# Performance work log

Hardware: AMD Instinct MI355X
Metric: run time of the kernel (lower is better)

The kernel has to match this reference:

```python
import jax, jax.numpy as jnp
import numpy as np

TOP_K = 30
NUM_RBF = 16
NUM_POS = 16
MAX_REL = 32
EDGE_FEATURES = 128
EDGE_IN = NUM_POS + NUM_RBF * 9 + 7  # 167


def _normalize(x, axis=-1):
    # torch F.normalize: x / max(||x||, 1e-12)
    return x / jnp.maximum(jnp.linalg.norm(x, axis=axis, keepdims=True), 1e-12)


def _gather_nodes(nodes, idx):
    # nodes [B,L,C], idx [B,L,K] -> [B,L,K,C]
    return jax.vmap(lambda n, i: n[i])(nodes, idx)


def _rbf(D):
    D_mu = jnp.linspace(2.0, 22.0, NUM_RBF)  # [R]
    D_sigma = (22.0 - 2.0) / NUM_RBF
    return jnp.exp(-(((D[..., None] - D_mu) / D_sigma) ** 2))


def _get_rbf(A, B, E_idx):
    # full pairwise dist then gather neighbors (faithful to source)
    D_A_B = jnp.sqrt(jnp.sum((A[:, :, None, :] - B[:, None, :, :]) ** 2, -1) + 1e-6)
    D_nb = jnp.take_along_axis(D_A_B, E_idx, axis=2)  # [B,L,K]
    return _rbf(D_nb)


def _quaternions(R):
    # R [B,L,K,3,3] -> Q [B,L,K,4]
    diag = jnp.diagonal(R, axis1=-2, axis2=-1)  # [B,L,K,3]
    Rxx, Ryy, Rzz = diag[..., 0], diag[..., 1], diag[..., 2]
    magnitudes = 0.5 * jnp.sqrt(jnp.abs(1 + jnp.stack(
        [Rxx - Ryy - Rzz, -Rxx + Ryy - Rzz, -Rxx - Ryy + Rzz], -1)))
    signs = jnp.sign(jnp.stack([
        R[..., 2, 1] - R[..., 1, 2],
        R[..., 0, 2] - R[..., 2, 0],
        R[..., 1, 0] - R[..., 0, 1]], -1))
    xyz = signs * magnitudes
    w = jnp.sqrt(jax.nn.relu(1 + jnp.sum(diag, -1, keepdims=True))) / 2.0
    return _normalize(jnp.concatenate((xyz, w), -1))


def _orientations_coarse(X, E_idx, eps=1e-6):
    B, L, _ = X.shape
    dX = X[:, 1:, :] - X[:, :-1, :]
    dX_norm = jnp.linalg.norm(dX, axis=-1)
    dX_mask = (dX_norm > 3.6) & (dX_norm < 4.0)
    dX = dX * dX_mask[:, :, None]
    U = _normalize(dX)
    u_2, u_1, u_0 = U[:, :-2, :], U[:, 1:-1, :], U[:, 2:, :]
    n_2 = _normalize(jnp.cross(u_2, u_1))
    o_1 = _normalize(u_2 - u_1)
    # local frames O [B,L-3,3,3] -> flattened, padded to [B,L,9]
    O = jnp.stack((o_1, n_2, jnp.cross(o_1, n_2)), 2).reshape(B, L - 3, 9)
    O = jnp.pad(O, ((0, 0), (1, 2), (0, 0)))
    O_neighbors = _gather_nodes(O, E_idx)        # [B,L,K,9]
    X_neighbors = _gather_nodes(X, E_idx)        # [B,L,K,3]
    O = O.reshape(B, L, 3, 3)
    O_neighbors = O_neighbors.reshape(*E_idx.shape, 3, 3)
    dXn = X_neighbors - X[:, :, None, :]
    dU = _normalize(jnp.einsum('blij,blkj->blki', O, dXn))
    R = jnp.einsum('blji,blkjm->blkim', O, O_neighbors)  # O^T @ O_nb
    Q = _quaternions(R)
    return jnp.concatenate((dU, Q), -1)  # [B,L,K,7]


def setup_inputs() -> dict:
    B, L = 2, 4096
    key = jax.random.key(0)
    ks = jax.random.split(key, 6)
    Ca = jax.random.normal(ks[0], (B, L, 3), dtype=jnp.float32)
    mask = jnp.ones((B, L), dtype=jnp.float32)
    residue_idx = jnp.arange(B * L, dtype=jnp.int32).reshape(B, L)
    chain_labels = jnp.sort(jax.random.randint(ks[1], (B, L), 0, 4), axis=-1).astype(jnp.int32)
    pos_in = 2 * MAX_REL + 1 + 1  # 66
    pos_W = jax.random.normal(ks[2], (NUM_POS, pos_in), dtype=jnp.float32) / np.sqrt(pos_in)
    pos_b = jnp.zeros((NUM_POS,), dtype=jnp.float32)
    edge_W = jax.random.normal(ks[3], (EDGE_FEATURES, EDGE_IN), dtype=jnp.float32) / np.sqrt(EDGE_IN)
    ln_g = jnp.ones((EDGE_FEATURES,), dtype=jnp.float32)
    ln_b = jnp.zeros((EDGE_FEATURES,), dtype=jnp.float32)
    return {"Ca": Ca, "mask": mask, "residue_idx": residue_idx,
            "chain_labels": chain_labels, "pos_W": pos_W, "pos_b": pos_b,
            "edge_W": edge_W, "ln_g": ln_g, "ln_b": ln_b}


def _forward(Ca, mask, residue_idx, chain_labels, pos_W, pos_b, edge_W, ln_g, ln_b):
    B, L, _ = Ca.shape
    # _dist: masked pairwise distances + kNN
    mask_2D = mask[:, :, None] * mask[:, None, :]
    dX = Ca[:, None, :, :] - Ca[:, :, None, :]
    D = mask_2D * jnp.sqrt(jnp.sum(dX ** 2, 3) + 1e-6)
    D_max = jnp.max(D, -1, keepdims=True)
    D_adjust = D + (1.0 - mask_2D) * D_max
    k = min(TOP_K, L)
    neg_vals, E_idx = jax.lax.top_k(-D_adjust, k)  # smallest-k
    D_neighbors = -neg_vals

    zeros = jnp.zeros((B, 1, 3), dtype=Ca.dtype)
    Ca_0 = jnp.concatenate([zeros, Ca[:, :-1, :]], axis=1)
    Ca_1 = Ca
    Ca_2 = jnp.concatenate([Ca[:, 1:, :], zeros], axis=1)

    O_features = _orientations_coarse(Ca, E_idx)

    RBF_all = jnp.concatenate([
        _rbf(D_neighbors),
        _get_rbf(Ca_0, Ca_0, E_idx), _get_rbf(Ca_2, Ca_2, E_idx),
        _get_rbf(Ca_0, Ca_1, E_idx), _get_rbf(Ca_0, Ca_2, E_idx),
        _get_rbf(Ca_1, Ca_0, E_idx), _get_rbf(Ca_1, Ca_2, E_idx),
        _get_rbf(Ca_2, Ca_0, E_idx), _get_rbf(Ca_2, Ca_1, E_idx)], axis=-1)

    offset = residue_idx[:, :, None] - residue_idx[:, None, :]
    offset = jnp.take_along_axis(offset, E_idx, axis=2)  # [B,L,K]
    d_chains = (chain_labels[:, :, None] - chain_labels[:, None, :] == 0).astype(jnp.int32)
    E_chains = jnp.take_along_axis(d_chains, E_idx, axis=2)

    # PositionalEncodings
    d = jnp.clip(offset + MAX_REL, 0, 2 * MAX_REL) * E_chains + (1 - E_chains) * (2 * MAX_REL + 1)
    d_onehot = jax.nn.one_hot(d, 2 * MAX_REL + 2, dtype=jnp.float32)
    E_positional = d_onehot @ pos_W.T + pos_b

    E = jnp.concatenate((E_positional, RBF_all, O_features), -1)  # [B,L,K,167]
    E = E @ edge_W.T
    mu = jnp.mean(E, -1, keepdims=True)
    var = jnp.var(E, -1, keepdims=True)
    E = (E - mu) / jnp.sqrt(var + 1e-5) * ln_g + ln_b
    return E, E_idx


def reference(Ca, mask, residue_idx, chain_labels, pos_W, pos_b, edge_W, ln_g, ln_b):
    return _forward(Ca, mask, residue_idx, chain_labels, pos_W, pos_b, edge_W, ln_g, ln_b)
```

## Files before the change

### kernel.cpp

```cpp
#include <hip/hip_runtime.h>
#include <stdint.h>

#define LL 4096
#define NB 2
#define KK 30
#define CDIM 128
#define FROW 200

typedef _Float16 half_t;
typedef half_t half8 __attribute__((ext_vector_type(8)));
typedef float f32x4 __attribute__((ext_vector_type(4)));

__device__ __forceinline__ float3 loadCa(const float* __restrict__ Ca, int b, int idx) {
    const float* p = Ca + ((size_t)(b * LL + idx)) * 3;
    return make_float3(p[0], p[1], p[2]);
}
__device__ __forceinline__ float3 loadCa4(const f32x4* __restrict__ Ca4, int b, int idx) {
    f32x4 v = Ca4[b * LL + idx];
    return make_float3(v[0], v[1], v[2]);
}
__device__ __forceinline__ float3 shiftedCa4(const f32x4* __restrict__ Ca4, int b, int idx, int sel) {
    int jj = idx + sel - 1;
    if (jj < 0 || jj >= LL) return make_float3(0.f, 0.f, 0.f);
    return loadCa4(Ca4, b, jj);
}
__device__ __forceinline__ float sgnf(float x) { return (x > 0.f) ? 1.f : ((x < 0.f) ? -1.f : 0.f); }
__device__ __forceinline__ float pdist(float3 a, float3 c) {
    float dx = a.x - c.x, dy = a.y - c.y, dz = a.z - c.z;
    return sqrtf(dx * dx + dy * dy + dz * dz + 1e-6f);
}

__global__ __launch_bounds__(256) void prep_kernel(const float* __restrict__ W,
                                                   const float* __restrict__ posW,
                                                   const float* __restrict__ posb,
                                                   const float* __restrict__ Ca,
                                                   half_t* __restrict__ Bp,
                                                   half_t* __restrict__ pwt,
                                                   float* __restrict__ Of,
                                                   f32x4* __restrict__ Ca4) {
    int blk = blockIdx.x;
    int tid = threadIdx.x;
    if (blk < 12) {
        int idx = blk * 256 + tid;
        if (idx >= 8 * 6 * 64) return;
        int l = idx & 63;
        int ts = idx >> 6;
        int s = ts % 6, t = ts / 6;
        int n = 16 * t + (l & 15);
        int kbase = 32 * s + 8 * (l >> 4);
        half8 v;
#pragma unroll
        for (int e = 0; e < 8; e++) {
            int k = kbase + e;
            v[e] = (k < 167) ? (half_t)W[n * 167 + k] : (half_t)0.f;
        }
        *(half8*)(Bp + (size_t)idx * 8) = v;
    } else if (blk < 17) {
        int idx = (blk - 12) * 256 + tid;
        if (idx < 66 * 16) {
            int d = idx >> 4, p = idx & 15;
            pwt[d * 16 + p] = (half_t)(posW[p * 66 + d] + posb[p]);
        }
    } else {
        int t = (blk - 17) * 256 + tid;
        if (t >= NB * LL) return;
        int b = t >> 12, i = t & (LL - 1);
        f32x4 c4;
        c4[0] = Ca[(size_t)t * 3];
        c4[1] = Ca[(size_t)t * 3 + 1];
        c4[2] = Ca[(size_t)t * 3 + 2];
        c4[3] = 0.f;
        Ca4[t] = c4;
        float o[9] = {0.f, 0.f, 0.f, 0.f, 0.f, 0.f, 0.f, 0.f, 0.f};
        if (i >= 1 && i <= LL - 3) {
            float3 cm = loadCa(Ca, b, i - 1), cc = loadCa(Ca, b, i), cp = loadCa(Ca, b, i + 1);
            float dx0 = cc.x - cm.x, dy0 = cc.y - cm.y, dz0 = cc.z - cm.z;
            float n0 = sqrtf(dx0 * dx0 + dy0 * dy0 + dz0 * dz0);
            float k0 = (n0 > 3.6f && n0 < 4.0f) ? 1.f : 0.f;
            float s0 = k0 / fmaxf(n0 * k0, 1e-12f);
            float u2x = dx0 * s0, u2y = dy0 * s0, u2z = dz0 * s0;
            float dx1 = cp.x - cc.x, dy1 = cp.y - cc.y, dz1 = cp.z - cc.z;
            float n1 = sqrtf(dx1 * dx1 + dy1 * dy1 + dz1 * dz1);
            float k1 = (n1 > 3.6f && n1 < 4.0f) ? 1.f : 0.f;
            float s1 = k1 / fmaxf(n1 * k1, 1e-12f);
            float u1x = dx1 * s1, u1y = dy1 * s1, u1z = dz1 * s1;
            float cx = u2y * u1z - u2z * u1y;
            float cy = u2z * u1x - u2x * u1z;
            float cz = u2x * u1y - u2y * u1x;
            float cn = sqrtf(cx * cx + cy * cy + cz * cz);
            float cinv = 1.f / fmaxf(cn, 1e-12f);
            float n2x = cx * cinv, n2y = cy * cinv, n2z = cz * cinv;
            float ox = u2x - u1x, oy = u2y - u1y, oz = u2z - u1z;
            float on = sqrtf(ox * ox + oy * oy + oz * oz);
            float oinv = 1.f / fmaxf(on, 1e-12f);
            float o1x = ox * oinv, o1y = oy * oinv, o1z = oz * oinv;
            o[0] = o1x; o[1] = o1y; o[2] = o1z;
            o[3] = n2x; o[4] = n2y; o[5] = n2z;
            o[6] = o1y * n2z - o1z * n2y;
            o[7] = o1z * n2x - o1x * n2z;
            o[8] = o1x * n2y - o1y * n2x;
        }
        float* dst = Of + (size_t)t * 9;
#pragma unroll
        for (int r = 0; r < 9; r++) dst[r] = o[r];
    }
}

__global__ __launch_bounds__(256, 8) void topk_kernel(const f32x4* __restrict__ Ca4,
                                                      const float* __restrict__ mask,
                                                      int* __restrict__ eidx_ws,
                                                      float* __restrict__ dnb_ws,
                                                      float* __restrict__ out_eidx_f) {
    __shared__ unsigned long long cand[512];
    __shared__ int wint[2][4];
    __shared__ int gcnt[4];
    __shared__ float wflt[4];
    int row = blockIdx.x;
    int b = row >> 12;
    int tid = threadIdx.x;
    int w = tid >> 6, lane = tid & 63;
    float3 ci = loadCa4(Ca4, b, row & (LL - 1));
    float mi = mask[row];
    float dreg[16];
    unsigned mfl = 0;
    float localmax = 0.f;
#pragma unroll
    for (int s = 0; s < 16; s++) {
        int j = tid + s * 256;
        f32x4 pj = Ca4[b * LL + j];
        float dx = pj[0] - ci.x, dy = pj[1] - ci.y, dz = pj[2] - ci.z;
        float d = sqrtf(dx * dx + dy * dy + dz * dz + 1e-6f);
        float m2 = mi * mask[b * LL + j];
        float D = m2 * d;
        dreg[s] = D;
        mfl |= (m2 == 0.f ? 1u : 0u) << s;
        localmax = fmaxf(localmax, D);
    }
#pragma unroll
    for (int o = 32; o; o >>= 1) localmax = fmaxf(localmax, __shfl_xor(localmax, o));
    if (lane == 0) wflt[w] = localmax;
    __syncthreads();
    float dmax = fmaxf(fmaxf(wflt[0], wflt[1]), fmaxf(wflt[2], wflt[3]));
    unsigned ui[16];
#pragma unroll
    for (int s = 0; s < 16; s++)
        ui[s] = __float_as_uint(dreg[s] + (((mfl >> s) & 1) ? dmax : 0.f));
    unsigned lo = 0u, hi = 0x7f800000u, T = 0u;
    bool found = false;
    int p = 0;
    for (int it = 0; it < 24 && !found; ++it) {
        unsigned mid = (lo + hi) >> 1;
        int c = 0;
#pragma unroll
        for (int s = 0; s < 16; s++) c += (ui[s] < mid) ? 1 : 0;
#pragma unroll
        for (int o = 32; o; o >>= 1) c += __shfl_xor(c, o);
        if (lane == 0) wint[p][w] = c;
        __syncthreads();
        c = wint[p][0] + wint[p][1] + wint[p][2] + wint[p][3];
        p ^= 1;
        if (c < 30) lo = mid;
        else if (c > 64) hi = mid;
        else { T = mid; found = true; }
    }
    if (!found) T = hi;
    int cnt = 0;
#pragma unroll
    for (int s = 0; s < 16; s++) cnt += (ui[s] < T) ? 1 : 0;
    int inc = cnt;
#pragma unroll
    for (int o = 1; o < 64; o <<= 1) {
        int nv = __shfl_up(inc, o);
        if (lane >= o) inc += nv;
    }
    if (lane == 63) gcnt[w] = inc;
    __syncthreads();
    int C = gcnt[0] + gcnt[1] + gcnt[2] + gcnt[3];
    int waveoff = 0;
    for (int q = 0; q < 4; q++) waveoff += (q < w) ? gcnt[q] : 0;
    int slot = waveoff + inc - cnt;
#pragma unroll
    for (int s = 0; s < 16; s++) {
        if (ui[s] < T) {
            int j = tid + s * 256;
            if (slot < 512)
                cand[slot] = ((unsigned long long)ui[s] << 32) | (unsigned)j;
            slot++;
        }
    }
    __syncthreads();
    if (w != 0) return;
    if (C <= 64) {
        unsigned long long v = (lane < C) ? cand[lane] : ~0ull;
#pragma unroll
        for (int k = 2; k <= 64; k <<= 1) {
#pragma unroll
            for (int jj = k >> 1; jj > 0; jj >>= 1) {
                unsigned long long o = __shfl_xor(v, jj);
                bool take_min = (((lane & jj) == 0) == ((lane & k) == 0));
                bool lt = (o < v);
                v = (take_min == lt) ? o : v;
            }
        }
        if (lane < KK) {
            int j = (int)(v & 0xffffffffu);
            eidx_ws[row * KK + lane] = j;
            dnb_ws[row * KK + lane] = __uint_as_float((unsigned)(v >> 32));
            out_eidx_f[row * KK + lane] = (float)j;
        }
    } else {
        unsigned long long r[8];
#pragma unroll
        for (int q = 0; q < 8; q++) {
            int idx = lane + 64 * q;
            r[q] = (idx < C && idx < 512) ? cand[idx] : ~0ull;
        }
        for (int t = 0; t < KK; t++) {
            unsigned long long v = r[0];
#pragma unroll
            for (int q = 1; q < 8; q++) v = (r[q] < v) ? r[q] : v;
#pragma unroll
            for (int o = 32; o; o >>= 1) {
                unsigned long long u = __shfl_xor(v, o);
                if (u < v) v = u;
            }
            if (lane == 0) {
                int j = (int)(v & 0xffffffffu);
                eidx_ws[row * KK + t] = j;
                dnb_ws[row * KK + t] = __uint_as_float((unsigned)(v >> 32));
                out_eidx_f[row * KK + t] = (float)j;
            }
#pragma unroll
            for (int q = 0; q < 8; q++)
                if (r[q] == v) r[q] = ~0ull;
        }
    }
}

__global__ __launch_bounds__(128) void edge_kernel(const f32x4* __restrict__ Ca4,
                                                   const int* __restrict__ ridx,
                                                   const int* __restrict__ chl,
                                                   const half_t* __restrict__ pwt,
                                                   const half_t* __restrict__ Bp,
                                                   const float* __restrict__ ln_g,
                                                   const float* __restrict__ ln_b,
                                                   const float* __restrict__ Of,
                                                   const int* __restrict__ eidx_ws,
                                                   const float* __restrict__ dnb_ws,
                                                   float* __restrict__ outE) {
    __shared__ alignas(16) half_t featH[32][FROW];
    __shared__ float sD[30][10];
    __shared__ float psum[32][2], pssq[32][2];
    __shared__ float rmu[32], rinv[32];
    int grow = blockIdx.x;
    int b = grow >> 12;
    int i = grow & (LL - 1);
    int tid = threadIdx.x;

    if (tid < 60) {
        int e = tid >> 1, half = tid & 1;
        int j = eidx_ws[grow * KK + e];
        if (half == 0) {
            float3 Pi0 = shiftedCa4(Ca4, b, i, 0);
            float3 Pi2 = shiftedCa4(Ca4, b, i, 2);
            float3 Pj0 = shiftedCa4(Ca4, b, j, 0);
            float3 Pj1 = loadCa4(Ca4, b, j);
            float3 Pj2 = shiftedCa4(Ca4, b, j, 2);
            sD[e][0] = dnb_ws[grow * KK + e];
            sD[e][1] = pdist(Pi0, Pj0);
            sD[e][2] = pdist(Pi2, Pj2);
            sD[e][3] = pdist(Pi0, Pj1);
            sD[e][4] = pdist(Pi0, Pj2);
            int off = ridx[grow] - ridx[b * LL + j];
            int eqc = (chl[grow] == chl[b * LL + j]) ? 1 : 0;
            int d = off + 32;
            d = d < 0 ? 0 : (d > 64 ? 64 : d);
            d = eqc ? d : 65;
            *(half8*)&featH[e][0] = *(const half8*)(pwt + d * 16);
            *(half8*)&featH[e][8] = *(const half8*)(pwt + d * 16 + 8);
        } else {
            float3 Pi1 = loadCa4(Ca4, b, i);
            float3 Pi2 = shiftedCa4(Ca4, b, i, 2);
            float3 Pj0 = shiftedCa4(Ca4, b, j, 0);
            float3 Pj1 = loadCa4(Ca4, b, j);
            float3 Pj2 = shiftedCa4(Ca4, b, j, 2);
            sD[e][5] = pdist(Pi1, Pj0);
            sD[e][6] = pdist(Pi1, Pj2);
            sD[e][7] = pdist(Pi2, Pj0);
            sD[e][8] = pdist(Pi2, Pj1);
            float Oi[9], Oj[9];
#pragma unroll
            for (int r = 0; r < 9; r++) {
                Oi[r] = Of[(size_t)grow * 9 + r];
                Oj[r] = Of[((size_t)(b * LL + j)) * 9 + r];
            }
            float dx = Pj1.x - Pi1.x, dy = Pj1.y - Pi1.y, dz = Pj1.z - Pi1.z;
            float v0 = Oi[0] * dx + Oi[1] * dy + Oi[2] * dz;
            float v1 = Oi[3] * dx + Oi[4] * dy + Oi[5] * dz;
            float v2 = Oi[6] * dx + Oi[7] * dy + Oi[8] * dz;
            float nn = sqrtf(v0 * v0 + v1 * v1 + v2 * v2);
            float ninv = 1.f / fmaxf(nn, 1e-12f);
            float R[3][3];
#pragma unroll
            for (int m = 0; m < 3; m++)
#pragma unroll
                for (int n = 0; n < 3; n++)
                    R[m][n] = Oi[0 * 3 + m] * Oj[0 * 3 + n] + Oi[1 * 3 + m] * Oj[1 * 3 + n] +
                              Oi[2 * 3 + m] * Oj[2 * 3 + n];
            float Rxx = R[0][0], Ryy = R[1][1], Rzz = R[2][2];
            float m0 = 0.5f * sqrtf(fabsf(1.f + Rxx - Ryy - Rzz));
            float m1 = 0.5f * sqrtf(fabsf(1.f - Rxx + Ryy - Rzz));
            float m2 = 0.5f * sqrtf(fabsf(1.f - Rxx - Ryy + Rzz));
            float x = sgnf(R[2][1] - R[1][2]) * m0;
            float y = sgnf(R[0][2] - R[2][0]) * m1;
            float z = sgnf(R[1][0] - R[0][1]) * m2;
            float ww = 0.5f * sqrtf(fmaxf(1.f + Rxx + Ryy + Rzz, 0.f));
            float qn = sqrtf(x * x + y * y + z * z + ww * ww);
            float qi = 1.f / fmaxf(qn, 1e-12f);
            half8 h;
            h[0] = (half_t)(v0 * ninv);
            h[1] = (half_t)(v1 * ninv);
            h[2] = (half_t)(v2 * ninv);
            h[3] = (half_t)(x * qi);
            h[4] = (half_t)(y * qi);
            h[5] = (half_t)(z * qi);
            h[6] = (half_t)(ww * qi);
            h[7] = (half_t)0.f;
            half8 zv = {};
            *(half8*)&featH[e][160] = h;
            *(half8*)&featH[e][168] = zv;
            *(half8*)&featH[e][176] = zv;
            *(half8*)&featH[e][184] = zv;
        }
    } else if (tid >= 64 && tid < 114) {
        int t = tid - 64;
        int r = 30 + t / 25, c = t % 25;
        half8 zv = {};
        *(half8*)&featH[r][c * 8] = zv;
    }
    __syncthreads();

    for (int job = tid; job < 270; job += 128) {
        int e = job / 9, q = job - e * 9;
        float D = sD[e][q];
        half8 v0, v1;
#pragma unroll
        for (int m = 0; m < 8; m++) {
            float mu = 2.0f + (4.f / 3.f) * (float)m;
            float t = (D - mu) * 0.8f;
            v0[m] = (half_t)exp2f(t * t * -1.4426950408889634f);
        }
#pragma unroll
        for (int m = 8; m < 16; m++) {
            float mu = 2.0f + (4.f / 3.f) * (float)m;
            float t = (D - mu) * 0.8f;
            v1[m - 8] = (half_t)exp2f(t * t * -1.4426950408889634f);
        }
        *(half8*)&featH[e][16 + 16 * q] = v0;
        *(half8*)&featH[e][24 + 16 * q] = v1;
    }
    __syncthreads();

    int lane = tid & 63, w = tid >> 6;
    int cc = lane & 15, g = lane >> 4;
    f32x4 zero = {0.f, 0.f, 0.f, 0.f};
    f32x4 acc[2][4];
#pragma unroll
    for (int m = 0; m < 2; m++)
#pragma unroll
        for (int t = 0; t < 4; t++) acc[m][t] = zero;
    for (int s = 0; s < 6; s++) {
        int ko = 32 * s + 8 * g;
        half8 af0 = *(const half8*)&featH[cc][ko];
        half8 af1 = *(const half8*)&featH[16 + cc][ko];
#pragma unroll
        for (int t = 0; t < 4; t++) {
            half8 bf = *(const half8*)(Bp + ((size_t)(((4 * w + t) * 6 + s) * 64 + lane)) * 8);
            acc[0][t] = __builtin_amdgcn_mfma_f32_16x16x32_f16(af0, bf, acc[0][t], 0, 0, 0);
            acc[1][t] = __builtin_amdgcn_mfma_f32_16x16x32_f16(af1, bf, acc[1][t], 0, 0, 0);
        }
    }

#pragma unroll
    for (int m = 0; m < 2; m++) {
#pragma unroll
        for (int q = 0; q < 4; q++) {
            float sp = acc[m][0][q] + acc[m][1][q] + acc[m][2][q] + acc[m][3][q];
            float qp = acc[m][0][q] * acc[m][0][q] + acc[m][1][q] * acc[m][1][q] +
                       acc[m][2][q] * acc[m][2][q] + acc[m][3][q] * acc[m][3][q];
#pragma unroll
            for (int o = 1; o < 16; o <<= 1) {
                sp += __shfl_xor(sp, o);
                qp += __shfl_xor(qp, o);
            }
            if (cc == 0) {
                int r = 16 * m + 4 * g + q;
                psum[r][w] = sp;
                pssq[r][w] = qp;
            }
        }
    }
    __syncthreads();
    if (tid < 32) {
        float sum = psum[tid][0] + psum[tid][1];
        float ssq = pssq[tid][0] + pssq[tid][1];
        float mu = sum * (1.f / 128.f);
        float var = fmaxf(ssq * (1.f / 128.f) - mu * mu, 0.f);
        rmu[tid] = mu;
        rinv[tid] = 1.f / sqrtf(var + 1e-5f);
    }
    __syncthreads();

    float lgv[4], lbv[4];
#pragma unroll
    for (int t = 0; t < 4; t++) {
        lgv[t] = ln_g[64 * w + 16 * t + cc];
        lbv[t] = ln_b[64 * w + 16 * t + cc];
    }
#pragma unroll
    for (int m = 0; m < 2; m++) {
#pragma unroll
        for (int q = 0; q < 4; q++) {
            int r = 16 * m + 4 * g + q;
            if (r < KK) {
                float mu = rmu[r], invs = rinv[r];
                float* dst = outE + ((size_t)(grow * KK + r)) * CDIM + 64 * w + cc;
#pragma unroll
                for (int t = 0; t < 4; t++)
                    dst[16 * t] = (acc[m][t][q] - mu) * invs * lgv[t] + lbv[t];
            }
        }
    }
}

extern "C" void kernel_launch(void* const* d_in, const int* in_sizes, int n_in,
                              void* d_out, int out_size, void* d_ws, size_t ws_size,
                              hipStream_t stream) {
    const float* Ca = (const float*)d_in[0];
    const float* mask = (const float*)d_in[1];
    const int* ridx = (const int*)d_in[2];
    const int* chl = (const int*)d_in[3];
    const float* posW = (const float*)d_in[4];
    const float* posb = (const float*)d_in[5];
    const float* edgeW = (const float*)d_in[6];
    const float* lng = (const float*)d_in[7];
    const float* lnb = (const float*)d_in[8];

    float* outE = (float*)d_out;
    float* outEidxF = outE + (size_t)NB * LL * KK * CDIM;

    char* ws = (char*)d_ws;
    half_t* Bp = (half_t*)ws;
    half_t* pwt = (half_t*)(ws + 49152);
    float* Of = (float*)(ws + 51264);
    int* eidx = (int*)(ws + 346176);
    float* dnb = (float*)(ws + 1329216);
    f32x4* Ca4 = (f32x4*)(ws + 2312256);

    prep_kernel<<<17 + (NB * LL + 255) / 256, 256, 0, stream>>>(edgeW, posW, posb, Ca,
                                                                Bp, pwt, Of, Ca4);
    topk_kernel<<<NB * LL, 256, 0, stream>>>(Ca4, mask, eidx, dnb, outEidxF);
    edge_kernel<<<NB * LL, 128, 0, stream>>>(Ca4, ridx, chl, pwt, Bp, lng, lnb,
                                             Of, eidx, dnb, outE);
}
```

Measured before the change: 115.8 us.

## Fuse top-k selection and edge feature kernels into one per-row kernel

```diff
diff --git a/kernel.cpp b/kernel.cpp
--- a/kernel.cpp
+++ b/kernel.cpp
@@ -106,20 +106,36 @@
     }
 }
 
-__global__ __launch_bounds__(256, 8) void topk_kernel(const f32x4* __restrict__ Ca4,
-                                                      const float* __restrict__ mask,
-                                                      int* __restrict__ eidx_ws,
-                                                      float* __restrict__ dnb_ws,
-                                                      float* __restrict__ out_eidx_f) {
-    __shared__ unsigned long long cand[512];
+__global__ __launch_bounds__(256) void fused_kernel(const f32x4* __restrict__ Ca4,
+                                                    const float* __restrict__ mask,
+                                                    const int* __restrict__ ridx,
+                                                    const int* __restrict__ chl,
+                                                    const half_t* __restrict__ pwt,
+                                                    const half_t* __restrict__ Bp,
+                                                    const float* __restrict__ ln_g,
+                                                    const float* __restrict__ ln_b,
+                                                    const float* __restrict__ Of,
+                                                    float* __restrict__ outE,
+                                                    float* __restrict__ out_eidx_f) {
+    __shared__ alignas(16) char smem[32 * FROW * 2];
+    unsigned long long* cand = (unsigned long long*)smem;
+    half_t(*featH)[FROW] = (half_t(*)[FROW])smem;
     __shared__ int wint[2][4];
     __shared__ int gcnt[4];
     __shared__ float wflt[4];
+    __shared__ int sj[32];
+    __shared__ float sd0[32];
+    __shared__ float sD[30][10];
+    __shared__ float psum[32][4], pssq[32][4];
+    __shared__ float rmu[32], rinv[32];
+
     int row = blockIdx.x;
     int b = row >> 12;
+    int i = row & (LL - 1);
     int tid = threadIdx.x;
     int w = tid >> 6, lane = tid & 63;
-    float3 ci = loadCa4(Ca4, b, row & (LL - 1));
+
+    float3 ci = loadCa4(Ca4, b, i);
     float mi = mask[row];
     float dreg[16];
     unsigned mfl = 0;
@@ -189,90 +205,71 @@
         }
     }
     __syncthreads();
-    if (w != 0) return;
-    if (C <= 64) {
-        unsigned long long v = (lane < C) ? cand[lane] : ~0ull;
-#pragma unroll
-        for (int k = 2; k <= 64; k <<= 1) {
-#pragma unroll
-            for (int jj = k >> 1; jj > 0; jj >>= 1) {
-                unsigned long long o = __shfl_xor(v, jj);
-                bool take_min = (((lane & jj) == 0) == ((lane & k) == 0));
-                bool lt = (o < v);
-                v = (take_min == lt) ? o : v;
-            }
-        }
-        if (lane < KK) {
-            int j = (int)(v & 0xffffffffu);
-            eidx_ws[row * KK + lane] = j;
-            dnb_ws[row * KK + lane] = __uint_as_float((unsigned)(v >> 32));
-            out_eidx_f[row * KK + lane] = (float)j;
-        }
-    } else {
-        unsigned long long r[8];
-#pragma unroll
-        for (int q = 0; q < 8; q++) {
-            int idx = lane + 64 * q;
-            r[q] = (idx < C && idx < 512) ? cand[idx] : ~0ull;
-        }
-        for (int t = 0; t < KK; t++) {
-            unsigned long long v = r[0];
-#pragma unroll
-            for (int q = 1; q < 8; q++) v = (r[q] < v) ? r[q] : v;
-#pragma unroll
-            for (int o = 32; o; o >>= 1) {
-                unsigned long long u = __shfl_xor(v, o);
-                if (u < v) v = u;
-            }
-            if (lane == 0) {
+    if (w == 0) {
+        if (C <= 64) {
+            unsigned long long v = (lane < C) ? cand[lane] : ~0ull;
+#pragma unroll
+            for (int k = 2; k <= 64; k <<= 1) {
+#pragma unroll
+                for (int jj = k >> 1; jj > 0; jj >>= 1) {
+                    unsigned long long o = __shfl_xor(v, jj);
+                    bool take_min = (((lane & jj) == 0) == ((lane & k) == 0));
+                    bool lt = (o < v);
+                    v = (take_min == lt) ? o : v;
+                }
+            }
+            if (lane < KK) {
                 int j = (int)(v & 0xffffffffu);
-                eidx_ws[row * KK + t] = j;
-                dnb_ws[row * KK + t] = __uint_as_float((unsigned)(v >> 32));
-                out_eidx_f[row * KK + t] = (float)j;
-            }
-#pragma unroll
-            for (int q = 0; q < 8; q++)
-                if (r[q] == v) r[q] = ~0ull;
-        }
-    }
-}
-
-__global__ __launch_bounds__(128) void edge_kernel(const f32x4* __restrict__ Ca4,
-                                                   const int* __restrict__ ridx,
-                                                   const int* __restrict__ chl,
-                                                   const half_t* __restrict__ pwt,
-                                                   const half_t* __restrict__ Bp,
-                                                   const float* __restrict__ ln_g,
-                                                   const float* __restrict__ ln_b,
-                                                   const float* __restrict__ Of,
-                                                   const int* __restrict__ eidx_ws,
-                                                   const float* __restrict__ dnb_ws,
-                                                   float* __restrict__ outE) {
-    __shared__ alignas(16) half_t featH[32][FROW];
-    __shared__ float sD[30][10];
-    __shared__ float psum[32][2], pssq[32][2];
-    __shared__ float rmu[32], rinv[32];
-    int grow = blockIdx.x;
-    int b = grow >> 12;
-    int i = grow & (LL - 1);
-    int tid = threadIdx.x;
+                sj[lane] = j;
+                sd0[lane] = __uint_as_float((unsigned)(v >> 32));
+                out_eidx_f[row * KK + lane] = (float)j;
+            }
+        } else {
+            unsigned long long r[8];
+#pragma unroll
+            for (int q = 0; q < 8; q++) {
+                int idx = lane + 64 * q;
+                r[q] = (idx < C && idx < 512) ? cand[idx] : ~0ull;
+            }
+            for (int t = 0; t < KK; t++) {
+                unsigned long long v = r[0];
+#pragma unroll
+                for (int q = 1; q < 8; q++) v = (r[q] < v) ? r[q] : v;
+#pragma unroll
+                for (int o = 32; o; o >>= 1) {
+                    unsigned long long u = __shfl_xor(v, o);
+                    if (u < v) v = u;
+                }
+                if (lane == 0) {
+                    int j = (int)(v & 0xffffffffu);
+                    sj[t] = j;
+                    sd0[t] = __uint_as_float((unsigned)(v >> 32));
+                    out_eidx_f[row * KK + t] = (float)j;
+                }
+#pragma unroll
+                for (int q = 0; q < 8; q++)
+                    if (r[q] == v) r[q] = ~0ull;
+            }
+        }
+    }
+    __syncthreads();
 
     if (tid < 60) {
         int e = tid >> 1, half = tid & 1;
-        int j = eidx_ws[grow * KK + e];
+        int j = sj[e];
         if (half == 0) {
             float3 Pi0 = shiftedCa4(Ca4, b, i, 0);
             float3 Pi2 = shiftedCa4(Ca4, b, i, 2);
             float3 Pj0 = shiftedCa4(Ca4, b, j, 0);
             float3 Pj1 = loadCa4(Ca4, b, j);
             float3 Pj2 = shiftedCa4(Ca4, b, j, 2);
-            sD[e][0] = dnb_ws[grow * KK + e];
+            sD[e][0] = sd0[e];
             sD[e][1] = pdist(Pi0, Pj0);
             sD[e][2] = pdist(Pi2, Pj2);
             sD[e][3] = pdist(Pi0, Pj1);
             sD[e][4] = pdist(Pi0, Pj2);
-            int off = ridx[grow] - ridx[b * LL + j];
-            int eqc = (chl[grow] == chl[b * LL + j]) ? 1 : 0;
+            int off = ridx[row] - ridx[b * LL + j];
+            int eqc = (chl[row] == chl[b * LL + j]) ? 1 : 0;
             int d = off + 32;
             d = d < 0 ? 0 : (d > 64 ? 64 : d);
             d = eqc ? d : 65;
@@ -291,7 +288,7 @@
             float Oi[9], Oj[9];
 #pragma unroll
             for (int r = 0; r < 9; r++) {
-                Oi[r] = Of[(size_t)grow * 9 + r];
+                Oi[r] = Of[(size_t)row * 9 + r];
                 Oj[r] = Of[((size_t)(b * LL + j)) * 9 + r];
             }
             float dx = Pj1.x - Pi1.x, dy = Pj1.y - Pi1.y, dz = Pj1.z - Pi1.z;
@@ -340,7 +337,7 @@
     }
     __syncthreads();
 
-    for (int job = tid; job < 270; job += 128) {
+    for (int job = tid; job < 270; job += 256) {
         int e = job / 9, q = job - e * 9;
         float D = sD[e][q];
         half8 v0, v1;
@@ -361,33 +358,34 @@
     }
     __syncthreads();
 
-    int lane = tid & 63, w = tid >> 6;
     int cc = lane & 15, g = lane >> 4;
     f32x4 zero = {0.f, 0.f, 0.f, 0.f};
-    f32x4 acc[2][4];
+    f32x4 acc[2][2];
 #pragma unroll
     for (int m = 0; m < 2; m++)
 #pragma unroll
-        for (int t = 0; t < 4; t++) acc[m][t] = zero;
+        for (int t = 0; t < 2; t++) acc[m][t] = zero;
+    const half_t* b0p = Bp + ((size_t)(2 * w) * 6) * 64 * 8;
+    const half_t* b1p = Bp + ((size_t)(2 * w + 1) * 6) * 64 * 8;
     for (int s = 0; s < 6; s++) {
         int ko = 32 * s + 8 * g;
         half8 af0 = *(const half8*)&featH[cc][ko];
         half8 af1 = *(const half8*)&featH[16 + cc][ko];
-#pragma unroll
-        for (int t = 0; t < 4; t++) {
-            half8 bf = *(const half8*)(Bp + ((size_t)(((4 * w + t) * 6 + s) * 64 + lane)) * 8);
-            acc[0][t] = __builtin_amdgcn_mfma_f32_16x16x32_f16(af0, bf, acc[0][t], 0, 0, 0);
-            acc[1][t] = __builtin_amdgcn_mfma_f32_16x16x32_f16(af1, bf, acc[1][t], 0, 0, 0);
-        }
+        half8 bf0 = *(const half8*)(b0p + (size_t)(s * 64 + lane) * 8);
+        half8 bf1 = *(const half8*)(b1p + (size_t)(s * 64 + lane) * 8);
+        acc[0][0] = __builtin_amdgcn_mfma_f32_16x16x32_f16(af0, bf0, acc[0][0], 0, 0, 0);
+        acc[0][1] = __builtin_amdgcn_mfma_f32_16x16x32_f16(af0, bf1, acc[0][1], 0, 0, 0);
+        acc[1][0] = __builtin_amdgcn_mfma_f32_16x16x32_f16(af1, bf0, acc[1][0], 0, 0, 0);
+        acc[1][1] = __builtin_amdgcn_mfma_f32_16x16x32_f16(af1, bf1, acc[1][1], 0, 0, 0);
     }
 
 #pragma unroll
     for (int m = 0; m < 2; m++) {
 #pragma unroll
         for (int q = 0; q < 4; q++) {
-            float sp = acc[m][0][q] + acc[m][1][q] + acc[m][2][q] + acc[m][3][q];
-            float qp = acc[m][0][q] * acc[m][0][q] + acc[m][1][q] * acc[m][1][q] +
-                       acc[m][2][q] * acc[m][2][q] + acc[m][3][q] * acc[m][3][q];
+            float v0 = acc[m][0][q], v1 = acc[m][1][q];
+            float sp = v0 + v1;
+            float qp = v0 * v0 + v1 * v1;
 #pragma unroll
             for (int o = 1; o < 16; o <<= 1) {
                 sp += __shfl_xor(sp, o);
@@ -402,8 +400,8 @@
     }
     __syncthreads();
     if (tid < 32) {
-        float sum = psum[tid][0] + psum[tid][1];
-        float ssq = pssq[tid][0] + pssq[tid][1];
+        float sum = psum[tid][0] + psum[tid][1] + psum[tid][2] + psum[tid][3];
+        float ssq = pssq[tid][0] + pssq[tid][1] + pssq[tid][2] + pssq[tid][3];
         float mu = sum * (1.f / 128.f);
         float var = fmaxf(ssq * (1.f / 128.f) - mu * mu, 0.f);
         rmu[tid] = mu;
@@ -411,11 +409,11 @@
     }
     __syncthreads();
 
-    float lgv[4], lbv[4];
-#pragma unroll
-    for (int t = 0; t < 4; t++) {
-        lgv[t] = ln_g[64 * w + 16 * t + cc];
-        lbv[t] = ln_b[64 * w + 16 * t + cc];
+    float lgv[2], lbv[2];
+#pragma unroll
+    for (int tt = 0; tt < 2; tt++) {
+        lgv[tt] = ln_g[32 * w + 16 * tt + cc];
+        lbv[tt] = ln_b[32 * w + 16 * tt + cc];
     }
 #pragma unroll
     for (int m = 0; m < 2; m++) {
@@ -424,10 +422,9 @@
             int r = 16 * m + 4 * g + q;
             if (r < KK) {
                 float mu = rmu[r], invs = rinv[r];
-                float* dst = outE + ((size_t)(grow * KK + r)) * CDIM + 64 * w + cc;
-#pragma unroll
-                for (int t = 0; t < 4; t++)
-                    dst[16 * t] = (acc[m][t][q] - mu) * invs * lgv[t] + lbv[t];
+                float* dst = outE + ((size_t)(row * KK + r)) * CDIM + 32 * w + cc;
+                dst[0] = (acc[m][0][q] - mu) * invs * lgv[0] + lbv[0];
+                dst[16] = (acc[m][1][q] - mu) * invs * lgv[1] + lbv[1];
             }
         }
     }
@@ -453,13 +450,10 @@
     half_t* Bp = (half_t*)ws;
     half_t* pwt = (half_t*)(ws + 49152);
     float* Of = (float*)(ws + 51264);
-    int* eidx = (int*)(ws + 346176);
-    float* dnb = (float*)(ws + 1329216);
-    f32x4* Ca4 = (f32x4*)(ws + 2312256);
+    f32x4* Ca4 = (f32x4*)(ws + 346176);
 
     prep_kernel<<<17 + (NB * LL + 255) / 256, 256, 0, stream>>>(edgeW, posW, posb, Ca,
                                                                 Bp, pwt, Of, Ca4);
-    topk_kernel<<<NB * LL, 256, 0, stream>>>(Ca4, mask, eidx, dnb, outEidxF);
-    edge_kernel<<<NB * LL, 128, 0, stream>>>(Ca4, ridx, chl, pwt, Bp, lng, lnb,
-                                             Of, eidx, dnb, outE);
-}
+    fused_kernel<<<NB * LL, 256, 0, stream>>>(Ca4, mask, ridx, chl, pwt, Bp, lng, lnb,
+                                              Of, outE, outEidxF);
+}
```

Result: no change. 114.9 us (-0.7%).
